# Kernel tuning notes

Measured on AMD Instinct MI355X. Metric: run time of the kernel, lower is better.

The kernel has to match this reference:

```python
import jax, jax.numpy as jnp
import numpy as np
from jax import lax

B, S, D = 4, 2048, 1024
E = 8           # num_experts
K = 2           # num_experts_per_tok (top-k)
F = 3264        # moe_intermediate_size = ceil(1024*pi/64)*64
NORM_TOPK = True


def setup_inputs() -> dict:
    key = jax.random.key(0)
    ks = jax.random.split(key, 8)
    sd = 0.02
    return {
        "x": jax.random.normal(ks[0], (B, S, D), jnp.float32),
        "gate_w": jax.random.normal(ks[1], (E, D), jnp.float32) * sd,
        "gate_b": jnp.zeros((E,), jnp.float32),
        "up_w": jax.random.normal(ks[2], (E, F, D), jnp.float32) * sd,
        "up_b": jnp.zeros((E, F), jnp.float32),
        "gp_w": jax.random.normal(ks[3], (E, F, D), jnp.float32) * sd,
        "gp_b": jnp.zeros((E, F), jnp.float32),
        "down_w": jax.random.normal(ks[4], (E, D, F), jnp.float32) * sd,
        "down_b": jnp.zeros((E, D), jnp.float32),
    }


def reference(x, gate_w, gate_b, up_w, up_b, gp_w, gp_b, down_w, down_b):
    bs, slen, dim = x.shape
    xf = x.reshape(-1, dim)                      # [N, D]
    N = xf.shape[0]

    # --- router: softmax over experts, top-k gating ---
    scores = jax.nn.softmax(xf @ gate_w.T + gate_b, axis=-1)   # [N, E]
    top_w, top_idx = lax.top_k(scores, K)                       # [N, K]
    if NORM_TOPK:
        top_w = top_w / (top_w.sum(-1, keepdims=True) + 1e-20)

    # per-(token, expert) combine weight: scatter top-k weights into [N, E]
    comb = jnp.zeros((N, E), xf.dtype).at[
        jnp.arange(N)[:, None], top_idx
    ].add(top_w)                                                # [N, E]

    # --- experts: y = sum_e comb[:, e] * FFN_e(x) (scan keeps memory O(N*F)) ---
    def step(acc, p):
        uw, ub, gw, gb, dw, db, w = p
        h = jax.nn.silu((xf @ gw.T + gb) * (xf @ uw.T + ub))    # [N, F]
        return acc + w[:, None] * (h @ dw.T + db), None

    y0 = jnp.zeros_like(xf)
    y, _ = lax.scan(step, y0, (up_w, up_b, gp_w, gp_b, down_w, down_b, comb.T))
    return y.reshape(bs, slen, dim)
```

## Files before the change

### kernel.cpp

```cpp
#include <hip/hip_runtime.h>
#include <cstdint>

#define NTOK 8192
#define DIM  1024
#define NEXP 8
#define NF   3264
#define NPAIR (NTOK*2)
#define TM 128
#define BK 64
#define ASTRIDE (BK+8)
#define MAXTILES 136

typedef __attribute__((ext_vector_type(8))) short short8;
typedef __attribute__((ext_vector_type(4))) float f32x4;

__device__ __forceinline__ unsigned short f2bf(float f){
    unsigned u = __float_as_uint(f);
    return (unsigned short)((u + 0x7FFFu + ((u >> 16) & 1u)) >> 16);
}
__device__ __forceinline__ unsigned pk2(float a, float b){
    return (unsigned)f2bf(a) | ((unsigned)f2bf(b) << 16);
}
__device__ __forceinline__ uint4 cvt8(const float* p){
    const float4* q = (const float4*)p;
    float4 a = q[0], b = q[1];
    uint4 r;
    r.x = pk2(a.x, a.y); r.y = pk2(a.z, a.w);
    r.z = pk2(b.x, b.y); r.w = pk2(b.z, b.w);
    return r;
}

__device__ __forceinline__ void gload16(const void* g, void* l){
    __builtin_amdgcn_global_load_lds(
        (const __attribute__((address_space(1))) unsigned int*)g,
        (__attribute__((address_space(3))) unsigned int*)l,
        16, 0, 0);
}

__global__ __launch_bounds__(256) void k_cvt(const float4* __restrict__ src,
                                             uint2* __restrict__ dst, int n4){
    int i = blockIdx.x * 256 + threadIdx.x;
    if (i >= n4) return;
    float4 a = src[i];
    uint2 r; r.x = pk2(a.x, a.y); r.y = pk2(a.z, a.w);
    dst[i] = r;
}

__global__ __launch_bounds__(256) void k_zero_f4(float4* __restrict__ p, int n4){
    int i = blockIdx.x * 256 + threadIdx.x;
    if (i < n4) p[i] = make_float4(0.f, 0.f, 0.f, 0.f);
}

__global__ void k_zero_ctrl(int* ctrl){
    if (threadIdx.x < 64) ctrl[threadIdx.x] = 0;
}

template<bool XB>
__global__ __launch_bounds__(256) void k_router(const float* __restrict__ x,
        const float* __restrict__ gw, const float* __restrict__ gb,
        int* __restrict__ top_idx, float* __restrict__ top_w, int* __restrict__ ctrl,
        unsigned short* __restrict__ xb){
    int wave = threadIdx.x >> 6;
    int lane = threadIdx.x & 63;
    int n = blockIdx.x * 4 + wave;
    const float* xr = x + (size_t)n * DIM;
    float acc[NEXP];
    #pragma unroll
    for (int e = 0; e < NEXP; e++) acc[e] = 0.f;
    for (int j = lane; j < DIM; j += 64){
        float xv = xr[j];
        if (XB) xb[(size_t)n * DIM + j] = f2bf(xv);
        #pragma unroll
        for (int e = 0; e < NEXP; e++) acc[e] += xv * gw[e * DIM + j];
    }
    #pragma unroll
    for (int e = 0; e < NEXP; e++){
        float v = acc[e];
        #pragma unroll
        for (int off = 32; off > 0; off >>= 1) v += __shfl_xor(v, off);
        acc[e] = v + gb[e];
    }
    if (lane == 0){
        int i0 = 0; float m0 = acc[0];
        #pragma unroll
        for (int e = 1; e < NEXP; e++) if (acc[e] > m0){ m0 = acc[e]; i0 = e; }
        int i1 = -1; float m1 = -3.4e38f;
        #pragma unroll
        for (int e = 0; e < NEXP; e++) if (e != i0 && acc[e] > m1){ m1 = acc[e]; i1 = e; }
        float b  = __expf(m1 - m0);
        float w0 = 1.f / (1.f + b);
        float w1 = b / (1.f + b);
        top_idx[n * 2] = i0; top_idx[n * 2 + 1] = i1;
        top_w[n * 2] = w0;  top_w[n * 2 + 1] = w1;
        atomicAdd(&ctrl[i0], 1);
        atomicAdd(&ctrl[i1], 1);
    }
}

__global__ void k_prefix(int* ctrl){
    int* counts = ctrl; int* offsets = ctrl + 8; int* tileOff = ctrl + 17; int* cursor = ctrl + 26;
    offsets[0] = 0; tileOff[0] = 0;
    for (int e = 0; e < NEXP; e++){
        offsets[e + 1] = offsets[e] + counts[e];
        tileOff[e + 1] = tileOff[e] + (counts[e] + TM - 1) / TM;
        cursor[e] = 0;
    }
}

__global__ __launch_bounds__(256) void k_scatter(const int* __restrict__ top_idx,
        const float* __restrict__ top_w, int* __restrict__ ctrl,
        int* __restrict__ pair_token, float* __restrict__ pair_w,
        int* __restrict__ inv_slot){
    const int* offsets = ctrl + 8;
    int* cursor = ctrl + 26;
    __shared__ int lcnt[NEXP];
    __shared__ int gbase[NEXP];
    int tid = threadIdx.x;
    if (tid < NEXP) lcnt[tid] = 0;
    __syncthreads();
    int n = blockIdx.x * 256 + tid;
    int e0 = top_idx[n * 2];
    int e1 = top_idx[n * 2 + 1];
    int p0 = atomicAdd(&lcnt[e0], 1);
    int p1 = atomicAdd(&lcnt[e1], 1);
    __syncthreads();
    if (tid < NEXP) gbase[tid] = atomicAdd(&cursor[tid], lcnt[tid]);
    __syncthreads();
    int s0 = offsets[e0] + gbase[e0] + p0;
    int s1 = offsets[e1] + gbase[e1] + p1;
    pair_token[s0] = n; pair_w[s0] = top_w[n * 2];
    pair_token[s1] = n; pair_w[s1] = top_w[n * 2 + 1];
    inv_slot[n * 2] = s0; inv_slot[n * 2 + 1] = s1;
}

__global__ __launch_bounds__(256) void k_combine(const float* __restrict__ ybuf,
        const int* __restrict__ inv_slot, float* __restrict__ out){
    int t = blockIdx.x;
    int c = threadIdx.x;
    int s0 = inv_slot[t * 2], s1 = inv_slot[t * 2 + 1];
    const float4* y0 = (const float4*)(ybuf + (size_t)s0 * DIM);
    const float4* y1 = (const float4*)(ybuf + (size_t)s1 * DIM);
    float4 a = y0[c], b = y1[c];
    float4 r = make_float4(a.x + b.x, a.y + b.y, a.z + b.z, a.w + b.w);
    ((float4*)(out + (size_t)t * DIM))[c] = r;
}


__global__ __launch_bounds__(256) void k_gemm1_dma(
        const unsigned short* __restrict__ xb,
        const unsigned short* __restrict__ wg, const unsigned short* __restrict__ wu,
        const float* __restrict__ gpb, const float* __restrict__ upb,
        const int* __restrict__ pair_token, const int* __restrict__ ctrl,
        unsigned short* __restrict__ hbuf){
    const int* offsets = ctrl + 8;
    const int* tileOff = ctrl + 17;
    int g = blockIdx.x;
    if (g >= tileOff[NEXP]) return;
    int e = 0;
    while (e < NEXP - 1 && g >= tileOff[e + 1]) e++;
    int row0 = (g - tileOff[e]) * TM;
    int nrows = offsets[e + 1] - offsets[e];
    int base_slot = offsets[e] + row0;
    int f0 = blockIdx.y * 64;
    int lt = blockIdx.x;

    __shared__ __align__(16) unsigned short As[TM][BK];
    __shared__ __align__(16) unsigned short Bs[TM][BK];

    int tid = threadIdx.x;
    int lane = tid & 63;
    int wave = __builtin_amdgcn_readfirstlane(tid >> 6);
    int rsub = lane >> 3;
    int cd = (lane & 7) ^ rsub;

    const unsigned short* a_g[4];
    const unsigned short* b_g[4];
    char* lA[4]; char* lB[4];
    #pragma unroll
    for (int j = 0; j < 4; j++){
        int chunk = wave * 4 + j;
        int row = chunk * 8 + rsub;
        int rr = (row0 + row < nrows) ? row : 0;
        int tok = pair_token[base_slot + rr] & (NTOK - 1);
        a_g[j] = xb + (size_t)tok * DIM + cd * 8;
        int f = f0 + ((row >> 5) << 4) + (row & 15);
        int up = (row >> 4) & 1;
        b_g[j] = (up ? wu : wg) + ((size_t)e * NF + f) * DIM + cd * 8;
        lA[j] = (char*)As + chunk * 1024;
        lB[j] = (char*)Bs + chunk * 1024;
    }

    int wr64 = (wave >> 1) * 64, wc = wave & 1;
    int lr = lane & 15, q = lane >> 4;
    int l7 = lr & 7;

    f32x4 acc[4][4];
    #pragma unroll
    for (int i = 0; i < 4; i++)
        #pragma unroll
        for (int j = 0; j < 4; j++) acc[i][j] = (f32x4){0.f, 0.f, 0.f, 0.f};

    for (int kb = 0; kb < DIM / BK; kb++){
        int k0 = kb * BK;
        #pragma unroll
        for (int j = 0; j < 4; j++) gload16(a_g[j] + k0, lA[j]);
        #pragma unroll
        for (int j = 0; j < 4; j++) gload16(b_g[j] + k0, lB[j]);
        __syncthreads();
        #pragma unroll
        for (int kk = 0; kk < 2; kk++){
            short8 av[4], bv[4];
            #pragma unroll
            for (int mf = 0; mf < 4; mf++){
                int row = wr64 + mf * 16 + lr;
                int c = kk * 4 + q;
                av[mf] = *(const short8*)((const char*)As + row * 128 + ((c ^ l7) * 16));
            }
            #pragma unroll
            for (int nf = 0; nf < 4; nf++){
                int row = wc * 64 + nf * 16 + lr;
                int c = kk * 4 + q;
                bv[nf] = *(const short8*)((const char*)Bs + row * 128 + ((c ^ l7) * 16));
            }
            #pragma unroll
            for (int mf = 0; mf < 4; mf++)
                #pragma unroll
                for (int nf = 0; nf < 4; nf++)
                    acc[mf][nf] = __builtin_amdgcn_mfma_f32_16x16x32_bf16(av[mf], bv[nf], acc[mf][nf], 0, 0, 0);
        }
        __syncthreads();
    }

    #pragma unroll
    for (int mf = 0; mf < 4; mf++){
        #pragma unroll
        for (int fp = 0; fp < 2; fp++){
            int fcol = f0 + (wc * 2 + fp) * 16 + lr;
            float gb_ = gpb[e * NF + fcol];
            float ub_ = upb[e * NF + fcol];
            #pragma unroll
            for (int r = 0; r < 4; r++){
                int m = wr64 + mf * 16 + q * 4 + r;
                if (row0 + m < nrows){
                    float gv = acc[mf][2 * fp][r] + gb_;
                    float uv = acc[mf][2 * fp + 1][r] + ub_;
                    float z = gv * uv;
                    float h = z / (1.f + __expf(-z));
                    hbuf[((size_t)(lt * TM + m)) * NF + fcol] = f2bf(h);
                }
            }
        }
    }
}

__global__ __launch_bounds__(256) void k_gemm2_dma(
        const unsigned short* __restrict__ hbuf,
        const unsigned short* __restrict__ wd, const float* __restrict__ db,
        const float* __restrict__ pair_w,
        const int* __restrict__ ctrl, float* __restrict__ ybuf){
    const int* offsets = ctrl + 8;
    const int* tileOff = ctrl + 17;
    int g = blockIdx.x;
    if (g >= tileOff[NEXP]) return;
    int e = 0;
    while (e < NEXP - 1 && g >= tileOff[e + 1]) e++;
    int row0 = (g - tileOff[e]) * TM;
    int nrows = offsets[e + 1] - offsets[e];
    int base_slot = offsets[e] + row0;
    int n0 = blockIdx.y * TM;
    int lt = blockIdx.x;

    __shared__ __align__(16) unsigned short As[TM][BK];
    __shared__ __align__(16) unsigned short Bs[TM][BK];

    int tid = threadIdx.x;
    int lane = tid & 63;
    int wave = __builtin_amdgcn_readfirstlane(tid >> 6);
    int rsub = lane >> 3;
    int cd = (lane & 7) ^ rsub;

    const unsigned short* a_g[4];
    const unsigned short* b_g[4];
    char* lA[4]; char* lB[4];
    #pragma unroll
    for (int j = 0; j < 4; j++){
        int chunk = wave * 4 + j;
        int row = chunk * 8 + rsub;
        a_g[j] = hbuf + ((size_t)(lt * TM + row)) * NF + cd * 8;
        int d = n0 + row;
        b_g[j] = wd + ((size_t)e * DIM + d) * NF + cd * 8;
        lA[j] = (char*)As + chunk * 1024;
        lB[j] = (char*)Bs + chunk * 1024;
    }

    int wr64 = (wave >> 1) * 64, wc = wave & 1, wc64 = (wave & 1) * 64;
    int lr = lane & 15, q = lane >> 4;
    int l7 = lr & 7;

    f32x4 acc[4][4];
    #pragma unroll
    for (int i = 0; i < 4; i++)
        #pragma unroll
        for (int j = 0; j < 4; j++) acc[i][j] = (f32x4){0.f, 0.f, 0.f, 0.f};

    for (int kb = 0; kb < NF / BK; kb++){
        int k0 = kb * BK;
        #pragma unroll
        for (int j = 0; j < 4; j++) gload16(a_g[j] + k0, lA[j]);
        #pragma unroll
        for (int j = 0; j < 4; j++) gload16(b_g[j] + k0, lB[j]);
        __syncthreads();
        #pragma unroll
        for (int kk = 0; kk < 2; kk++){
            short8 av[4], bv[4];
            #pragma unroll
            for (int mf = 0; mf < 4; mf++){
                int row = wr64 + mf * 16 + lr;
                int c = kk * 4 + q;
                av[mf] = *(const short8*)((const char*)As + row * 128 + ((c ^ l7) * 16));
            }
            #pragma unroll
            for (int nf = 0; nf < 4; nf++){
                int row = wc64 + nf * 16 + lr;
                int c = kk * 4 + q;
                bv[nf] = *(const short8*)((const char*)Bs + row * 128 + ((c ^ l7) * 16));
            }
            #pragma unroll
            for (int mf = 0; mf < 4; mf++)
                #pragma unroll
                for (int nf = 0; nf < 4; nf++)
                    acc[mf][nf] = __builtin_amdgcn_mfma_f32_16x16x32_bf16(av[mf], bv[nf], acc[mf][nf], 0, 0, 0);
        }
        __syncthreads();
    }

    #pragma unroll
    for (int mf = 0; mf < 4; mf++){
        #pragma unroll
        for (int r = 0; r < 4; r++){
            int m = wr64 + mf * 16 + q * 4 + r;
            if (row0 + m < nrows){
                int slot = base_slot + m;
                float w = pair_w[slot];
                float* yr = ybuf + (size_t)slot * DIM;
                #pragma unroll
                for (int nf = 0; nf < 4; nf++){
                    int n = n0 + wc * 64 + nf * 16 + lr;
                    yr[n] = w * (acc[mf][nf][r] + db[e * DIM + n]);
                }
            }
        }
    }
}

template<bool WB, bool XB>
__global__ __launch_bounds__(256) void k_gemm1(
        const float* __restrict__ xf, const unsigned short* __restrict__ xb,
        const unsigned short* __restrict__ wg, const unsigned short* __restrict__ wu,
        const float* __restrict__ wgf, const float* __restrict__ wuf,
        const float* __restrict__ gpb, const float* __restrict__ upb,
        const int* __restrict__ pair_token, const int* __restrict__ ctrl,
        unsigned short* __restrict__ hbuf, int t0){
    const int* offsets = ctrl + 8;
    const int* tileOff = ctrl + 17;
    int g = t0 + blockIdx.x;
    if (g >= tileOff[NEXP]) return;
    int e = 0;
    while (e < NEXP - 1 && g >= tileOff[e + 1]) e++;
    int row0 = (g - tileOff[e]) * TM;
    int nrows = offsets[e + 1] - offsets[e];
    int base_slot = offsets[e] + row0;
    int f0 = blockIdx.y * 64;
    int lt = blockIdx.x;

    __shared__ unsigned short As[TM][ASTRIDE];
    __shared__ unsigned short Bs[TM][ASTRIDE];

    int tid = threadIdx.x;
    int sr = tid >> 3, sc = tid & 7;

    const unsigned short* a_src[4];
    const float* a_srcf[4];
    bool a_val[4];
    #pragma unroll
    for (int it = 0; it < 4; it++){
        int r = it * 32 + sr;
        bool v = (row0 + r) < nrows;
        int tok = v ? (pair_token[base_slot + r] & (NTOK - 1)) : 0;
        a_val[it] = v;
        if (XB) a_src[it]  = xb + (size_t)tok * DIM + sc * 8;
        else    a_srcf[it] = xf + (size_t)tok * DIM + sc * 8;
    }
    const unsigned short* b_src[4];
    const float* b_srcf[4];
    #pragma unroll
    for (int it = 0; it < 4; it++){
        int br = it * 32 + sr;
        int f = f0 + ((br >> 5) << 4) + (br & 15);
        bool up = (br >> 4) & 1;
        size_t woff = ((size_t)e * NF + f) * DIM + sc * 8;
        if (WB) b_src[it]  = (up ? wu : wg) + woff;
        else    b_srcf[it] = (up ? wuf : wgf) + woff;
    }

    int lane = tid & 63, wave = tid >> 6;
    int wr64 = (wave >> 1) * 64, wc = wave & 1, wc64 = wc * 64;
    int lr = lane & 15, q = lane >> 4;

    f32x4 acc[4][4];
    #pragma unroll
    for (int i = 0; i < 4; i++)
        #pragma unroll
        for (int j = 0; j < 4; j++) acc[i][j] = (f32x4){0.f, 0.f, 0.f, 0.f};

    for (int kb = 0; kb < DIM / BK; kb++){
        int k0 = kb * BK;
        #pragma unroll
        for (int it = 0; it < 4; it++){
            uint4 v = make_uint4(0u, 0u, 0u, 0u);
            if (a_val[it]){
                if (XB) v = *(const uint4*)(a_src[it] + k0);
                else    v = cvt8(a_srcf[it] + k0);
            }
            *(uint4*)&As[it * 32 + sr][sc * 8] = v;
        }
        #pragma unroll
        for (int it = 0; it < 4; it++){
            uint4 v;
            if (WB) v = *(const uint4*)(b_src[it] + k0);
            else    v = cvt8(b_srcf[it] + k0);
            *(uint4*)&Bs[it * 32 + sr][sc * 8] = v;
        }
        __syncthreads();
        #pragma unroll
        for (int kk = 0; kk < 2; kk++){
            short8 av[4], bv[4];
            #pragma unroll
            for (int mf = 0; mf < 4; mf++) av[mf] = *(const short8*)&As[wr64 + mf * 16 + lr][kk * 32 + q * 8];
            #pragma unroll
            for (int nf = 0; nf < 4; nf++) bv[nf] = *(const short8*)&Bs[wc64 + nf * 16 + lr][kk * 32 + q * 8];
            #pragma unroll
            for (int mf = 0; mf < 4; mf++)
                #pragma unroll
                for (int nf = 0; nf < 4; nf++)
                    acc[mf][nf] = __builtin_amdgcn_mfma_f32_16x16x32_bf16(av[mf], bv[nf], acc[mf][nf], 0, 0, 0);
        }
        __syncthreads();
    }

    #pragma unroll
    for (int mf = 0; mf < 4; mf++){
        #pragma unroll
        for (int fp = 0; fp < 2; fp++){
            int fcol = f0 + (wc * 2 + fp) * 16 + lr;
            float gb_ = gpb[e * NF + fcol];
            float ub_ = upb[e * NF + fcol];
            #pragma unroll
            for (int r = 0; r < 4; r++){
                int m = wr64 + mf * 16 + q * 4 + r;
                if (row0 + m < nrows){
                    float gv = acc[mf][2 * fp][r] + gb_;
                    float uv = acc[mf][2 * fp + 1][r] + ub_;
                    float z = gv * uv;
                    float h = z / (1.f + __expf(-z));
                    hbuf[((size_t)(lt * TM + m)) * NF + fcol] = f2bf(h);
                }
            }
        }
    }
}

template<bool WB>
__global__ __launch_bounds__(256) void k_gemm2(
        const unsigned short* __restrict__ hbuf,
        const unsigned short* __restrict__ wd, const float* __restrict__ wdf,
        const float* __restrict__ db,
        const int* __restrict__ pair_token, const float* __restrict__ pair_w,
        const int* __restrict__ ctrl, float* __restrict__ out, int t0){
    const int* offsets = ctrl + 8;
    const int* tileOff = ctrl + 17;
    int g = t0 + blockIdx.x;
    if (g >= tileOff[NEXP]) return;
    int e = 0;
    while (e < NEXP - 1 && g >= tileOff[e + 1]) e++;
    int row0 = (g - tileOff[e]) * TM;
    int nrows = offsets[e + 1] - offsets[e];
    int base_slot = offsets[e] + row0;
    int n0 = blockIdx.y * TM;
    int lt = blockIdx.x;

    __shared__ unsigned short As[TM][ASTRIDE];
    __shared__ unsigned short Bs[TM][ASTRIDE];

    int tid = threadIdx.x;
    int sr = tid >> 3, sc = tid & 7;

    const unsigned short* a_src[4]; bool a_val[4];
    #pragma unroll
    for (int it = 0; it < 4; it++){
        int r = it * 32 + sr;
        a_val[it] = (row0 + r) < nrows;
        a_src[it] = hbuf + ((size_t)(lt * TM + r)) * NF + sc * 8;
    }
    const unsigned short* b_src[4];
    const float* b_srcf[4];
    #pragma unroll
    for (int it = 0; it < 4; it++){
        int d = n0 + it * 32 + sr;
        size_t woff = ((size_t)e * DIM + d) * NF + sc * 8;
        if (WB) b_src[it]  = wd + woff;
        else    b_srcf[it] = wdf + woff;
    }

    int lane = tid & 63, wave = tid >> 6;
    int wr64 = (wave >> 1) * 64, wc = wave & 1, wc64 = wc * 64;
    int lr = lane & 15, q = lane >> 4;

    f32x4 acc[4][4];
    #pragma unroll
    for (int i = 0; i < 4; i++)
        #pragma unroll
        for (int j = 0; j < 4; j++) acc[i][j] = (f32x4){0.f, 0.f, 0.f, 0.f};

    for (int kb = 0; kb < NF / BK; kb++){
        int k0 = kb * BK;
        #pragma unroll
        for (int it = 0; it < 4; it++){
            uint4 v = make_uint4(0u, 0u, 0u, 0u);
            if (a_val[it]) v = *(const uint4*)(a_src[it] + k0);
            *(uint4*)&As[it * 32 + sr][sc * 8] = v;
        }
        #pragma unroll
        for (int it = 0; it < 4; it++){
            uint4 v;
            if (WB) v = *(const uint4*)(b_src[it] + k0);
            else    v = cvt8(b_srcf[it] + k0);
            *(uint4*)&Bs[it * 32 + sr][sc * 8] = v;
        }
        __syncthreads();
        #pragma unroll
        for (int kk = 0; kk < 2; kk++){
            short8 av[4], bv[4];
            #pragma unroll
            for (int mf = 0; mf < 4; mf++) av[mf] = *(const short8*)&As[wr64 + mf * 16 + lr][kk * 32 + q * 8];
            #pragma unroll
            for (int nf = 0; nf < 4; nf++) bv[nf] = *(const short8*)&Bs[wc64 + nf * 16 + lr][kk * 32 + q * 8];
            #pragma unroll
            for (int mf = 0; mf < 4; mf++)
                #pragma unroll
                for (int nf = 0; nf < 4; nf++)
                    acc[mf][nf] = __builtin_amdgcn_mfma_f32_16x16x32_bf16(av[mf], bv[nf], acc[mf][nf], 0, 0, 0);
        }
        __syncthreads();
    }

    #pragma unroll
    for (int mf = 0; mf < 4; mf++){
        #pragma unroll
        for (int r = 0; r < 4; r++){
            int m = wr64 + mf * 16 + q * 4 + r;
            if (row0 + m < nrows){
                int slot = base_slot + m;
                int tok = pair_token[slot] & (NTOK - 1);
                float w = pair_w[slot];
                #pragma unroll
                for (int nf = 0; nf < 4; nf++){
                    int n = n0 + wc64 + nf * 16 + lr;
                    float v = w * (acc[mf][nf][r] + db[e * DIM + n]);
                    atomicAdd(&out[(size_t)tok * DIM + n], v);
                }
            }
        }
    }
}

extern "C" void kernel_launch(void* const* d_in, const int* in_sizes, int n_in,
                              void* d_out, int out_size, void* d_ws, size_t ws_size,
                              hipStream_t stream){
    (void)in_sizes; (void)n_in; (void)out_size;
    const float* x      = (const float*)d_in[0];
    const float* gate_w = (const float*)d_in[1];
    const float* gate_b = (const float*)d_in[2];
    const float* up_w   = (const float*)d_in[3];
    const float* up_b   = (const float*)d_in[4];
    const float* gp_w   = (const float*)d_in[5];
    const float* gp_b   = (const float*)d_in[6];
    const float* down_w = (const float*)d_in[7];
    const float* down_b = (const float*)d_in[8];
    float* out = (float*)d_out;
    char* ws = (char*)d_ws;

    const size_t SZ_XB   = (size_t)NTOK * DIM * 2;
    const size_t SZ_W    = (size_t)NEXP * NF * DIM * 2;
    const size_t TILE_SZ = (size_t)TM * NF * 2;

    size_t off = 0;
    int*   ctrl       = (int*)(ws + off);   off += 256;
    int*   pair_token = (int*)(ws + off);   off += (size_t)NPAIR * 4;
    float* pair_w     = (float*)(ws + off); off += (size_t)NPAIR * 4;
    int*   top_idx    = (int*)(ws + off);   off += (size_t)NTOK * 2 * 4;
    float* top_w      = (float*)(ws + off); off += (size_t)NTOK * 2 * 4;
    int*   inv_slot   = (int*)(ws + off);   off += (size_t)NTOK * 2 * 4;

    size_t rem = (ws_size > off) ? (ws_size - off) : 0;
    bool XB = false, WB = false;
    unsigned short* xb = nullptr;
    unsigned short *wg = nullptr, *wu = nullptr, *wd = nullptr;

    if (rem >= SZ_XB + TILE_SZ){
        XB = true;
        xb = (unsigned short*)(ws + off); off += SZ_XB; rem -= SZ_XB;
    }
    if (rem >= 3 * SZ_W + (size_t)MAXTILES * TILE_SZ){
        WB = true;
        wg = (unsigned short*)(ws + off); off += SZ_W;
        wu = (unsigned short*)(ws + off); off += SZ_W;
        wd = (unsigned short*)(ws + off); off += SZ_W;
        rem -= 3 * SZ_W;
    }
    int TC = (int)((rem / TILE_SZ) < (size_t)MAXTILES ? (rem / TILE_SZ) : (size_t)MAXTILES);
    if (TC < 1) TC = 1;
    unsigned short* hbuf = (unsigned short*)(ws + off);
    int NCH = (MAXTILES + TC - 1) / TC;
    bool FAST = XB && WB && (TC == MAXTILES);
    float* ybuf = (float*)wg;

    int out_n4 = NTOK * DIM / 4;
    k_zero_ctrl<<<1, 64, 0, stream>>>(ctrl);
    if (WB){
        int n4 = NEXP * NF * DIM / 4;
        int gc = (n4 + 255) / 256;
        k_cvt<<<gc, 256, 0, stream>>>((const float4*)gp_w,   (uint2*)wg, n4);
        k_cvt<<<gc, 256, 0, stream>>>((const float4*)up_w,   (uint2*)wu, n4);
        k_cvt<<<gc, 256, 0, stream>>>((const float4*)down_w, (uint2*)wd, n4);
    }
    if (XB) k_router<true ><<<NTOK / 4, 256, 0, stream>>>(x, gate_w, gate_b, top_idx, top_w, ctrl, xb);
    else    k_router<false><<<NTOK / 4, 256, 0, stream>>>(x, gate_w, gate_b, top_idx, top_w, ctrl, xb);
    k_prefix<<<1, 1, 0, stream>>>(ctrl);
    k_scatter<<<NTOK / 256, 256, 0, stream>>>(top_idx, top_w, ctrl, pair_token, pair_w, inv_slot);

    if (FAST){
        dim3 g1(MAXTILES, NF / 64);
        dim3 g2(MAXTILES, DIM / TM);
        k_gemm1_dma<<<g1, 256, 0, stream>>>(xb, wg, wu, gp_b, up_b, pair_token, ctrl, hbuf);
        k_gemm2_dma<<<g2, 256, 0, stream>>>(hbuf, wd, down_b, pair_w, ctrl, ybuf);
        k_combine<<<NTOK, 256, 0, stream>>>(ybuf, inv_slot, out);
    } else {
        k_zero_f4<<<(out_n4 + 255) / 256, 256, 0, stream>>>((float4*)out, out_n4);
        dim3 g1((unsigned)TC, NF / 64);
        dim3 g2((unsigned)TC, DIM / TM);
        for (int c = 0; c < NCH; c++){
            int t0 = c * TC;
            if (WB){
                if (XB) k_gemm1<true, true ><<<g1, 256, 0, stream>>>(x, xb, wg, wu, nullptr, nullptr, gp_b, up_b, pair_token, ctrl, hbuf, t0);
                else    k_gemm1<true, false><<<g1, 256, 0, stream>>>(x, xb, wg, wu, nullptr, nullptr, gp_b, up_b, pair_token, ctrl, hbuf, t0);
                k_gemm2<true ><<<g2, 256, 0, stream>>>(hbuf, wd, nullptr, down_b, pair_token, pair_w, ctrl, out, t0);
            } else {
                if (XB) k_gemm1<false, true ><<<g1, 256, 0, stream>>>(x, xb, nullptr, nullptr, gp_w, up_w, gp_b, up_b, pair_token, ctrl, hbuf, t0);
                else    k_gemm1<false, false><<<g1, 256, 0, stream>>>(x, xb, nullptr, nullptr, gp_w, up_w, gp_b, up_b, pair_token, ctrl, hbuf, t0);
                k_gemm2<false><<<g2, 256, 0, stream>>>(hbuf, nullptr, down_w, down_b, pair_token, pair_w, ctrl, out, t0);
            }
        }
    }
}
```

Measured before the change: 1.017 ms.

## Split-K gemm2 over two partial buffers, fuse weight conversion, drop prefix kernel

The down-projection GEMM gets a split-K variant: blockIdx.z halves the K range and each half writes its partial result to its own fp32 buffer. The combine kernel sums both halves, which doubles the grid to improve CU occupancy. The three weight conversion launches become one kernel. The prefix-sum kernel is removed, and each GEMM block now recomputes its tile offsets from the expert counts. This costs extra partial-buffer traffic and workspace, and the split path runs only when the workspace is large enough.

```diff
diff --git a/kernel.cpp b/kernel.cpp
--- a/kernel.cpp
+++ b/kernel.cpp
@@ -10,6 +10,7 @@
 #define BK 64
 #define ASTRIDE (BK+8)
 #define MAXTILES 136
+#define N4W (NEXP*NF*DIM/4)
 
 typedef __attribute__((ext_vector_type(8))) short short8;
 typedef __attribute__((ext_vector_type(4))) float f32x4;
@@ -37,13 +38,35 @@
         16, 0, 0);
 }
 
-__global__ __launch_bounds__(256) void k_cvt(const float4* __restrict__ src,
-                                             uint2* __restrict__ dst, int n4){
+__device__ __forceinline__ bool tile_lookup(const int* __restrict__ counts, int g,
+        int& e, int& row0, int& nrows, int& base_slot){
+    e = -1;
+    int toff = 0, ooff = 0;
+    #pragma unroll
+    for (int i = 0; i < NEXP; i++){
+        int c = counts[i];
+        int nt = (c + TM - 1) / TM;
+        if (e < 0 && g < toff + nt){
+            e = i; row0 = (g - toff) * TM; nrows = c; base_slot = ooff + row0;
+        }
+        toff += nt; ooff += c;
+    }
+    return e >= 0;
+}
+
+__global__ __launch_bounds__(256) void k_cvt3(
+        const float4* __restrict__ s0, const float4* __restrict__ s1,
+        const float4* __restrict__ s2,
+        uint2* __restrict__ d0, uint2* __restrict__ d1, uint2* __restrict__ d2){
     int i = blockIdx.x * 256 + threadIdx.x;
-    if (i >= n4) return;
-    float4 a = src[i];
+    if (i >= 3 * N4W) return;
+    int t = i / N4W;
+    int j = i - t * N4W;
+    const float4* s = (t == 0) ? s0 : (t == 1) ? s1 : s2;
+    uint2* d = (t == 0) ? d0 : (t == 1) ? d1 : d2;
+    float4 a = s[j];
     uint2 r; r.x = pk2(a.x, a.y); r.y = pk2(a.z, a.w);
-    dst[i] = r;
+    d[j] = r;
 }
 
 __global__ __launch_bounds__(256) void k_zero_f4(float4* __restrict__ p, int n4){
@@ -97,24 +120,14 @@
     }
 }
 
-__global__ void k_prefix(int* ctrl){
-    int* counts = ctrl; int* offsets = ctrl + 8; int* tileOff = ctrl + 17; int* cursor = ctrl + 26;
-    offsets[0] = 0; tileOff[0] = 0;
-    for (int e = 0; e < NEXP; e++){
-        offsets[e + 1] = offsets[e] + counts[e];
-        tileOff[e + 1] = tileOff[e] + (counts[e] + TM - 1) / TM;
-        cursor[e] = 0;
-    }
-}
-
 __global__ __launch_bounds__(256) void k_scatter(const int* __restrict__ top_idx,
         const float* __restrict__ top_w, int* __restrict__ ctrl,
         int* __restrict__ pair_token, float* __restrict__ pair_w,
         int* __restrict__ inv_slot){
-    const int* offsets = ctrl + 8;
-    int* cursor = ctrl + 26;
+    int* cursor = ctrl + 8;
     __shared__ int lcnt[NEXP];
     __shared__ int gbase[NEXP];
+    __shared__ int soff[NEXP];
     int tid = threadIdx.x;
     if (tid < NEXP) lcnt[tid] = 0;
     __syncthreads();
@@ -124,27 +137,36 @@
     int p0 = atomicAdd(&lcnt[e0], 1);
     int p1 = atomicAdd(&lcnt[e1], 1);
     __syncthreads();
-    if (tid < NEXP) gbase[tid] = atomicAdd(&cursor[tid], lcnt[tid]);
+    if (tid < NEXP){
+        gbase[tid] = atomicAdd(&cursor[tid], lcnt[tid]);
+        int off = 0;
+        for (int i = 0; i < tid; i++) off += ctrl[i];
+        soff[tid] = off;
+    }
     __syncthreads();
-    int s0 = offsets[e0] + gbase[e0] + p0;
-    int s1 = offsets[e1] + gbase[e1] + p1;
+    int s0 = soff[e0] + gbase[e0] + p0;
+    int s1 = soff[e1] + gbase[e1] + p1;
     pair_token[s0] = n; pair_w[s0] = top_w[n * 2];
     pair_token[s1] = n; pair_w[s1] = top_w[n * 2 + 1];
     inv_slot[n * 2] = s0; inv_slot[n * 2 + 1] = s1;
 }
 
+template<int NZ>
 __global__ __launch_bounds__(256) void k_combine(const float* __restrict__ ybuf,
         const int* __restrict__ inv_slot, float* __restrict__ out){
     int t = blockIdx.x;
     int c = threadIdx.x;
     int s0 = inv_slot[t * 2], s1 = inv_slot[t * 2 + 1];
-    const float4* y0 = (const float4*)(ybuf + (size_t)s0 * DIM);
-    const float4* y1 = (const float4*)(ybuf + (size_t)s1 * DIM);
-    float4 a = y0[c], b = y1[c];
-    float4 r = make_float4(a.x + b.x, a.y + b.y, a.z + b.z, a.w + b.w);
+    float4 r = make_float4(0.f, 0.f, 0.f, 0.f);
+    #pragma unroll
+    for (int z = 0; z < NZ; z++){
+        const float* base = ybuf + (size_t)z * NPAIR * DIM;
+        float4 a = ((const float4*)(base + (size_t)s0 * DIM))[c];
+        float4 b = ((const float4*)(base + (size_t)s1 * DIM))[c];
+        r.x += a.x + b.x; r.y += a.y + b.y; r.z += a.z + b.z; r.w += a.w + b.w;
+    }
     ((float4*)(out + (size_t)t * DIM))[c] = r;
 }
-
 
 __global__ __launch_bounds__(256) void k_gemm1_dma(
         const unsigned short* __restrict__ xb,
@@ -152,15 +174,9 @@
         const float* __restrict__ gpb, const float* __restrict__ upb,
         const int* __restrict__ pair_token, const int* __restrict__ ctrl,
         unsigned short* __restrict__ hbuf){
-    const int* offsets = ctrl + 8;
-    const int* tileOff = ctrl + 17;
     int g = blockIdx.x;
-    if (g >= tileOff[NEXP]) return;
-    int e = 0;
-    while (e < NEXP - 1 && g >= tileOff[e + 1]) e++;
-    int row0 = (g - tileOff[e]) * TM;
-    int nrows = offsets[e + 1] - offsets[e];
-    int base_slot = offsets[e] + row0;
+    int e, row0, nrows, base_slot;
+    if (!tile_lookup(ctrl, g, e, row0, nrows, base_slot)) return;
     int f0 = blockIdx.y * 64;
     int lt = blockIdx.x;
 
@@ -253,22 +269,22 @@
     }
 }
 
+template<int NZ>
 __global__ __launch_bounds__(256) void k_gemm2_dma(
         const unsigned short* __restrict__ hbuf,
         const unsigned short* __restrict__ wd, const float* __restrict__ db,
         const float* __restrict__ pair_w,
         const int* __restrict__ ctrl, float* __restrict__ ybuf){
-    const int* offsets = ctrl + 8;
-    const int* tileOff = ctrl + 17;
     int g = blockIdx.x;
-    if (g >= tileOff[NEXP]) return;
-    int e = 0;
-    while (e < NEXP - 1 && g >= tileOff[e + 1]) e++;
-    int row0 = (g - tileOff[e]) * TM;
-    int nrows = offsets[e + 1] - offsets[e];
-    int base_slot = offsets[e] + row0;
+    int e, row0, nrows, base_slot;
+    if (!tile_lookup(ctrl, g, e, row0, nrows, base_slot)) return;
     int n0 = blockIdx.y * TM;
     int lt = blockIdx.x;
+    int z = (NZ > 1) ? blockIdx.z : 0;
+    const int KBT = NF / BK;
+    const int KCH = (KBT + NZ - 1) / NZ;
+    int kb0 = z * KCH;
+    int kb1 = (kb0 + KCH < KBT) ? (kb0 + KCH) : KBT;
 
     __shared__ __align__(16) unsigned short As[TM][BK];
     __shared__ __align__(16) unsigned short Bs[TM][BK];
@@ -303,7 +319,7 @@
         #pragma unroll
         for (int j = 0; j < 4; j++) acc[i][j] = (f32x4){0.f, 0.f, 0.f, 0.f};
 
-    for (int kb = 0; kb < NF / BK; kb++){
+    for (int kb = kb0; kb < kb1; kb++){
         int k0 = kb * BK;
         #pragma unroll
         for (int j = 0; j < 4; j++) gload16(a_g[j] + k0, lA[j]);
@@ -334,6 +350,7 @@
         __syncthreads();
     }
 
+    float* yz = ybuf + (size_t)z * NPAIR * DIM;
     #pragma unroll
     for (int mf = 0; mf < 4; mf++){
         #pragma unroll
@@ -342,11 +359,12 @@
             if (row0 + m < nrows){
                 int slot = base_slot + m;
                 float w = pair_w[slot];
-                float* yr = ybuf + (size_t)slot * DIM;
+                float* yr = yz + (size_t)slot * DIM;
                 #pragma unroll
                 for (int nf = 0; nf < 4; nf++){
                     int n = n0 + wc * 64 + nf * 16 + lr;
-                    yr[n] = w * (acc[mf][nf][r] + db[e * DIM + n]);
+                    float bterm = (z == 0) ? db[e * DIM + n] : 0.f;
+                    yr[n] = w * (acc[mf][nf][r] + bterm);
                 }
             }
         }
@@ -361,15 +379,9 @@
         const float* __restrict__ gpb, const float* __restrict__ upb,
         const int* __restrict__ pair_token, const int* __restrict__ ctrl,
         unsigned short* __restrict__ hbuf, int t0){
-    const int* offsets = ctrl + 8;
-    const int* tileOff = ctrl + 17;
     int g = t0 + blockIdx.x;
-    if (g >= tileOff[NEXP]) return;
-    int e = 0;
-    while (e < NEXP - 1 && g >= tileOff[e + 1]) e++;
-    int row0 = (g - tileOff[e]) * TM;
-    int nrows = offsets[e + 1] - offsets[e];
-    int base_slot = offsets[e] + row0;
+    int e, row0, nrows, base_slot;
+    if (!tile_lookup(ctrl, g, e, row0, nrows, base_slot)) return;
     int f0 = blockIdx.y * 64;
     int lt = blockIdx.x;
 
@@ -477,15 +489,9 @@
         const float* __restrict__ db,
         const int* __restrict__ pair_token, const float* __restrict__ pair_w,
         const int* __restrict__ ctrl, float* __restrict__ out, int t0){
-    const int* offsets = ctrl + 8;
-    const int* tileOff = ctrl + 17;
     int g = t0 + blockIdx.x;
-    if (g >= tileOff[NEXP]) return;
-    int e = 0;
-    while (e < NEXP - 1 && g >= tileOff[e + 1]) e++;
-    int row0 = (g - tileOff[e]) * TM;
-    int nrows = offsets[e + 1] - offsets[e];
-    int base_slot = offsets[e] + row0;
+    int e, row0, nrows, base_slot;
+    if (!tile_lookup(ctrl, g, e, row0, nrows, base_slot)) return;
     int n0 = blockIdx.y * TM;
     int lt = blockIdx.x;
 
@@ -592,6 +598,7 @@
 
     const size_t SZ_XB   = (size_t)NTOK * DIM * 2;
     const size_t SZ_W    = (size_t)NEXP * NF * DIM * 2;
+    const size_t SZ_Y    = (size_t)NPAIR * DIM * 4;
     const size_t TILE_SZ = (size_t)TM * NF * 2;
 
     size_t off = 0;
@@ -623,28 +630,33 @@
     unsigned short* hbuf = (unsigned short*)(ws + off);
     int NCH = (MAXTILES + TC - 1) / TC;
     bool FAST = XB && WB && (TC == MAXTILES);
-    float* ybuf = (float*)wg;
+    size_t off_end = off + (size_t)MAXTILES * TILE_SZ;
+    bool FAST2 = FAST && (ws_size >= off_end + 2 * SZ_Y);
+    float* ybuf1 = (float*)wg;
+    float* ybuf2 = (float*)(ws + off_end);
 
     int out_n4 = NTOK * DIM / 4;
     k_zero_ctrl<<<1, 64, 0, stream>>>(ctrl);
     if (WB){
-        int n4 = NEXP * NF * DIM / 4;
-        int gc = (n4 + 255) / 256;
-        k_cvt<<<gc, 256, 0, stream>>>((const float4*)gp_w,   (uint2*)wg, n4);
-        k_cvt<<<gc, 256, 0, stream>>>((const float4*)up_w,   (uint2*)wu, n4);
-        k_cvt<<<gc, 256, 0, stream>>>((const float4*)down_w, (uint2*)wd, n4);
+        int gc = (3 * N4W + 255) / 256;
+        k_cvt3<<<gc, 256, 0, stream>>>((const float4*)gp_w, (const float4*)up_w,
+                                       (const float4*)down_w,
+                                       (uint2*)wg, (uint2*)wu, (uint2*)wd);
     }
     if (XB) k_router<true ><<<NTOK / 4, 256, 0, stream>>>(x, gate_w, gate_b, top_idx, top_w, ctrl, xb);
     else    k_router<false><<<NTOK / 4, 256, 0, stream>>>(x, gate_w, gate_b, top_idx, top_w, ctrl, xb);
-    k_prefix<<<1, 1, 0, stream>>>(ctrl);
     k_scatter<<<NTOK / 256, 256, 0, stream>>>(top_idx, top_w, ctrl, pair_token, pair_w, inv_slot);
 
     if (FAST){
         dim3 g1(MAXTILES, NF / 64);
-        dim3 g2(MAXTILES, DIM / TM);
         k_gemm1_dma<<<g1, 256, 0, stream>>>(xb, wg, wu, gp_b, up_b, pair_token, ctrl, hbuf);
-        k_gemm2_dma<<<g2, 256, 0, stream>>>(hbuf, wd, down_b, pair_w, ctrl, ybuf);
-        k_combine<<<NTOK, 256, 0, stream>>>(ybuf, inv_slot, out);
+        if (FAST2){
+            k_gemm2_dma<2><<<dim3(MAXTILES, DIM / TM, 2), 256, 0, stream>>>(hbuf, wd, down_b, pair_w, ctrl, ybuf2);
+            k_combine<2><<<NTOK, 256, 0, stream>>>(ybuf2, inv_slot, out);
+        } else {
+            k_gemm2_dma<1><<<dim3(MAXTILES, DIM / TM, 1), 256, 0, stream>>>(hbuf, wd, down_b, pair_w, ctrl, ybuf1);
+            k_combine<1><<<NTOK, 256, 0, stream>>>(ybuf1, inv_slot, out);
+        }
     } else {
         k_zero_f4<<<(out_n4 + 255) / 256, 256, 0, stream>>>((float4*)out, out_n4);
         dim3 g1((unsigned)TC, NF / 64);
```

Result: no change. 1.024 ms (+0.6%).
